# Kernel optimization log

Measured on AMD Instinct MI355X. Metric: run time of the kernel, lower is better.

The kernel has to match this reference:

```python
import jax, jax.numpy as jnp
import numpy as np

EPS = 1e-5

def _face_normals(v, vi):
    # v: [B,V,3], vi: [F,3] -> [B,F,3]
    pts = v[:, vi]                                  # [B,F,3,3]
    n = jnp.cross(pts[:, :, 1] - pts[:, :, 0], pts[:, :, 2] - pts[:, :, 0])
    norm = jnp.linalg.norm(n, axis=-1, keepdims=True)
    return n / jnp.where(norm < EPS, 1.0, norm)

def _vert_normals(v, vi):
    fn = _face_normals(v, vi)                       # [B,F,3]
    fn_rep = jnp.repeat(fn, 3, axis=1)              # [B,3F,3] (one copy per face vertex)
    vn = jnp.zeros_like(v).at[:, vi.reshape(-1)].add(fn_rep)
    norm = jnp.linalg.norm(vn, axis=-1, keepdims=True)
    return vn / jnp.where(norm < EPS, 1.0, norm)

def _values_to_uv(values, index_image, bary_image):
    # values: [B,V,C]; index_image/bary_image: [U,U,3] -> [B,C,U,U]
    mask = jnp.all(index_image != -1, axis=-1)      # [U,U]
    idx = jnp.clip(index_image, 0, values.shape[1] - 1)
    vals = values[:, idx]                           # [B,U,U,3,C]
    uv = jnp.einsum('buvkc,uvk->bcuv', vals, bary_image.astype(values.dtype))
    return uv * mask[None, None].astype(values.dtype)

def _grid_sample_bilinear(img, gx, gy):
    # img: [B,C,H,W]; gx,gy: [N] in [-1,1]; align_corners=False, zero padding
    B, C, H, W = img.shape
    ix = ((gx + 1.0) * W - 1.0) * 0.5
    iy = ((gy + 1.0) * H - 1.0) * 0.5
    x0 = jnp.floor(ix); y0 = jnp.floor(iy)
    x1 = x0 + 1.0;      y1 = y0 + 1.0
    wx1 = ix - x0; wx0 = 1.0 - wx1
    wy1 = iy - y0; wy0 = 1.0 - wy1
    def gather(xi, yi):
        valid = (xi >= 0) & (xi < W) & (yi >= 0) & (yi < H)
        xc = jnp.clip(xi, 0, W - 1).astype(jnp.int32)
        yc = jnp.clip(yi, 0, H - 1).astype(jnp.int32)
        return img[:, :, yc, xc] * valid.astype(img.dtype)  # [B,C,N]
    return (gather(x0, y0) * (wx0 * wy0) + gather(x1, y0) * (wx1 * wy0)
          + gather(x0, y1) * (wx0 * wy1) + gather(x1, y1) * (wx1 * wy1))

def _sample_uv(values_uv, uv_coords, v2uv):
    g = uv_coords * 2.0 - 1.0                       # [T,2]
    vals = _grid_sample_bilinear(values_uv, g[:, 0], g[:, 1])  # [B,C,T]
    vals = jnp.transpose(vals, (0, 2, 1))           # [B,T,C]
    return vals[:, v2uv].mean(axis=2)               # [B,V,C]

def setup_inputs() -> dict:
    key = jax.random.key(0)
    ks = jax.random.split(key, 6)
    B, V, Fc, U, T, K = 8, 100000, 200000, 1024, 110000, 2
    verts = jax.random.normal(ks[0], (B, V, 3), jnp.float32)
    vi = jax.random.randint(ks[1], (Fc, 3), 0, V, dtype=jnp.int32)
    index_image = jax.random.randint(ks[2], (U, U, 3), 0, V, dtype=jnp.int32)
    bary_image = jax.random.uniform(ks[3], (U, U, 3), jnp.float32)
    vt = jax.random.uniform(ks[4], (T, 2), jnp.float32)
    v2uv = jax.random.randint(ks[5], (V, K), 0, T, dtype=jnp.int32)
    return {"verts": verts, "bary_image": bary_image, "vt": vt,
            "vi": vi, "index_image": index_image, "v2uv": v2uv}

def reference(verts, bary_image, vt, vi, index_image, v2uv):
    vn = _vert_normals(verts, vi)                   # [B,V,3]
    uv = _values_to_uv(vn, index_image, bary_image) # [B,3,U,U]
    return _sample_uv(uv, vt, v2uv)                 # [B,V,3]
```

## Files before the change

kernel.cpp:

```cpp
#include <hip/hip_runtime.h>

#define EPS 1e-5f

constexpr int B = 8;
constexpr int V = 100000;
constexpr int F = 200000;
constexpr int U = 1024;
constexpr int T = 110000;
constexpr int CAP = 24;

constexpr int TRB = (V + 255) / 256;
constexpr int CZB = (V + 255) / 256;

constexpr int N4   = (3 * F) / 4;
constexpr int ELLB = (N4 + 255) / 256;
constexpr int FNB  = (F * 8 + 255) / 256;
constexpr int CPB  = (T + 255) / 256;
constexpr int PERIODS = ELLB;
constexpr int K2N = PERIODS * 17;

__global__ void k1_pre(const float* __restrict__ verts,
                       float4* __restrict__ vertsT,
                       int* __restrict__ cnt) {
    int blk = blockIdx.x;
    if (blk < TRB) {
        int v = blk * 256 + threadIdx.x;
        if (v >= V) return;
        float4 row[8];
#pragma unroll
        for (int b = 0; b < 8; ++b) {
            const float* p = verts + (size_t)b * V * 3 + (size_t)v * 3;
            row[b] = make_float4(p[0], p[1], p[2], 0.0f);
        }
        float4* dst = vertsT + (size_t)v * 8;
#pragma unroll
        for (int b = 0; b < 8; ++b) dst[b] = row[b];
    } else {
        int i = (blk - TRB) * 256 + threadIdx.x;
        if (i < V) cnt[i] = 0;
    }
}

__global__ void k2_fused(const int* __restrict__ vi,
                         int* __restrict__ cnt,
                         int* __restrict__ ell,
                         const float4* __restrict__ vertsT,
                         float4* __restrict__ fn,
                         const int* __restrict__ index_image,
                         const float* __restrict__ bary_image,
                         const float* __restrict__ vt,
                         int4* __restrict__ cI,
                         float4* __restrict__ cW) {
    int p = blockIdx.x / 17;
    int s = blockIdx.x % 17;

    if (s == 0) {
        int m4 = p * 256 + threadIdx.x;
        if (m4 >= N4) return;
        const int4* vi4 = (const int4*)vi;
        int4 e = vi4[m4];
        int base = m4 * 4;
        int vv[4] = {e.x, e.y, e.z, e.w};
#pragma unroll
        for (int j = 0; j < 4; ++j) {
            int v = vv[j];
            int pos = atomicAdd(&cnt[v], 1);
            if (pos < CAP) ell[v * CAP + pos] = (base + j) / 3;
        }
        return;
    }

    if (s <= 15) {
        int bid = p * 15 + (s - 1);
        if (bid >= FNB) return;
        int id = bid * 256 + threadIdx.x;
        if (id >= F * 8) return;
        int f = id >> 3;
        int b = id & 7;

        int i0 = vi[f * 3 + 0];
        int i1 = vi[f * 3 + 1];
        int i2 = vi[f * 3 + 2];

        float4 p0 = vertsT[(size_t)i0 * 8 + b];
        float4 p1 = vertsT[(size_t)i1 * 8 + b];
        float4 p2 = vertsT[(size_t)i2 * 8 + b];

        float e1x = p1.x - p0.x, e1y = p1.y - p0.y, e1z = p1.z - p0.z;
        float e2x = p2.x - p0.x, e2y = p2.y - p0.y, e2z = p2.z - p0.z;

        float nx = e1y * e2z - e1z * e2y;
        float ny = e1z * e2x - e1x * e2z;
        float nz = e1x * e2y - e1y * e2x;

        float norm = sqrtf(nx * nx + ny * ny + nz * nz);
        float inv = (norm < EPS) ? 1.0f : (1.0f / norm);
        fn[id] = make_float4(nx * inv, ny * inv, nz * inv, 0.0f);
        return;
    }

    if (p >= CPB) return;
    int t = p * 256 + threadIdx.x;
    if (t >= T) return;

    float gx = vt[t * 2 + 0];
    float gy = vt[t * 2 + 1];
    float ix = gx * (float)U - 0.5f;
    float iy = gy * (float)U - 0.5f;

    float x0f = floorf(ix);
    float y0f = floorf(iy);
    int x0 = (int)x0f;
    int y0 = (int)y0f;
    float wx1 = ix - x0f, wx0 = 1.0f - wx1;
    float wy1 = iy - y0f, wy0 = 1.0f - wy1;

#pragma unroll
    for (int c = 0; c < 4; ++c) {
        int cy = c >> 1, cx = c & 1;
        int y = y0 + cy;
        int x = x0 + cx;
        int4 ci = make_int4(0, 0, 0, 0);
        float4 cw = make_float4(0.0f, 0.0f, 0.0f, 0.0f);
        if (x >= 0 && x < U && y >= 0 && y < U) {
            float w = (cy ? wy1 : wy0) * (cx ? wx1 : wx0);
            int pix = y * U + x;
            int i0 = index_image[pix * 3 + 0];
            int i1 = index_image[pix * 3 + 1];
            int i2 = index_image[pix * 3 + 2];
            float m = (i0 != -1 && i1 != -1 && i2 != -1) ? 1.0f : 0.0f;
            float wm = w * m;
            ci.x = min(max(i0, 0), V - 1);
            ci.y = min(max(i1, 0), V - 1);
            ci.z = min(max(i2, 0), V - 1);
            cw.x = wm * bary_image[pix * 3 + 0];
            cw.y = wm * bary_image[pix * 3 + 1];
            cw.z = wm * bary_image[pix * 3 + 2];
        }
        cI[t * 4 + c] = ci;
        cW[t * 4 + c] = cw;
    }
}

__global__ void gather_vn(const float4* __restrict__ fn,
                          const int* __restrict__ cnt,
                          const int* __restrict__ ell,
                          float4* __restrict__ vn) {
    int id = blockIdx.x * blockDim.x + threadIdx.x;
    if (id >= V * 8) return;
    int v = id >> 3;
    int b = id & 7;

    int deg = min(cnt[v], CAP);
    const int* row = ell + (size_t)v * CAP;

    float ax = 0.0f, ay = 0.0f, az = 0.0f;
    for (int j = 0; j < deg; ++j) {
        int f = row[j];
        float4 n = fn[(size_t)f * 8 + b];
        ax += n.x; ay += n.y; az += n.z;
    }

    float n = sqrtf(ax * ax + ay * ay + az * az);
    float inv = (n < EPS) ? 1.0f : (1.0f / n);
    vn[id] = make_float4(ax * inv, ay * inv, az * inv, 0.0f);
}

__global__ void sample_points(const float4* __restrict__ vn,
                              const int4* __restrict__ cI,
                              const float4* __restrict__ cW,
                              float4* __restrict__ vals) {
    int id = blockIdx.x * blockDim.x + threadIdx.x;
    if (id >= T * 8) return;
    int t = id >> 3;
    int b = id & 7;

    float ax = 0.0f, ay = 0.0f, az = 0.0f;
#pragma unroll
    for (int c = 0; c < 4; ++c) {
        int4 ci = cI[t * 4 + c];
        float4 cw = cW[t * 4 + c];
        float4 q0 = vn[(size_t)ci.x * 8 + b];
        float4 q1 = vn[(size_t)ci.y * 8 + b];
        float4 q2 = vn[(size_t)ci.z * 8 + b];
        ax += cw.x * q0.x + cw.y * q1.x + cw.z * q2.x;
        ay += cw.x * q0.y + cw.y * q1.y + cw.z * q2.y;
        az += cw.x * q0.z + cw.y * q1.z + cw.z * q2.z;
    }

    vals[id] = make_float4(ax, ay, az, 0.0f);
}

__global__ void gather_out(const float4* __restrict__ vals,
                           const int* __restrict__ v2uv,
                           float* __restrict__ out) {
    int id = blockIdx.x * blockDim.x + threadIdx.x;
    if (id >= V * 8) return;
    int v = id >> 3;
    int b = id & 7;

    int t0 = v2uv[v * 2 + 0];
    int t1 = v2uv[v * 2 + 1];
    float4 x = vals[(size_t)t0 * 8 + b];
    float4 y = vals[(size_t)t1 * 8 + b];

    float* o = out + (size_t)b * V * 3 + (size_t)v * 3;
    o[0] = 0.5f * (x.x + y.x);
    o[1] = 0.5f * (x.y + y.y);
    o[2] = 0.5f * (x.z + y.z);
}

extern "C" void kernel_launch(void* const* d_in, const int* in_sizes, int n_in,
                              void* d_out, int out_size, void* d_ws, size_t ws_size,
                              hipStream_t stream) {
    const float* verts   = (const float*)d_in[0];
    const float* bary    = (const float*)d_in[1];
    const float* vt      = (const float*)d_in[2];
    const int*   vi      = (const int*)d_in[3];
    const int*   idx_img = (const int*)d_in[4];
    const int*   v2uv    = (const int*)d_in[5];
    float* out = (float*)d_out;

    float4* vertsT = (float4*)d_ws;
    float4* vn     = vertsT;
    float4* fn     = vertsT + (size_t)V * 8;
    float4* vals   = fn;
    int4*   cI     = (int4*)(fn + (size_t)F * 8);
    float4* cW     = (float4*)(cI + (size_t)T * 4);
    int*    cnt    = (int*)(cW + (size_t)T * 4);
    int*    ell    = cnt + V;

    const int BLK = 256;
    k1_pre<<<TRB + CZB, BLK, 0, stream>>>(verts, vertsT, cnt);
    k2_fused<<<K2N, BLK, 0, stream>>>(
        vi, cnt, ell, vertsT, fn, idx_img, bary, vt, cI, cW);
    gather_vn<<<(V * 8 + BLK - 1) / BLK, BLK, 0, stream>>>(fn, cnt, ell, vn);
    sample_points<<<(T * 8 + BLK - 1) / BLK, BLK, 0, stream>>>(vn, cI, cW, vals);
    gather_out<<<(V * 8 + BLK - 1) / BLK, BLK, 0, stream>>>(vals, v2uv, out);
}
```

Before: 195.9 us.

## Replace global-atomic ELL build with bucketed counting-sort adjacency and shared-memory gather

Replaces the per-vertex global atomicAdd ELL construction with a two-pass bucketed counting sort. Per-block shared-memory histograms are built over 128-vertex buckets, scanned into offsets, and used to scatter packed (local vertex, face) pairs. Each bucket block then rebuilds its adjacency rows in shared memory and gathers the face normals. This removes contended global atomics and scattered ELL writes, at the cost of two extra kernel launches, a serial single-block scan, and nondeterministic face ordering within rows.

```diff
diff --git a/kernel.cpp b/kernel.cpp
--- a/kernel.cpp
+++ b/kernel.cpp
@@ -9,19 +9,18 @@
 constexpr int T = 110000;
 constexpr int CAP = 24;
 
-constexpr int TRB = (V + 255) / 256;
-constexpr int CZB = (V + 255) / 256;
-
+constexpr int NBUK = (V + 127) / 128;
 constexpr int N4   = (3 * F) / 4;
-constexpr int ELLB = (N4 + 255) / 256;
+constexpr int EB   = (N4 + 255) / 256;
+constexpr int TRB  = (V + 255) / 256;
 constexpr int FNB  = (F * 8 + 255) / 256;
 constexpr int CPB  = (T + 255) / 256;
-constexpr int PERIODS = ELLB;
-constexpr int K2N = PERIODS * 17;
 
 __global__ void k1_pre(const float* __restrict__ verts,
                        float4* __restrict__ vertsT,
-                       int* __restrict__ cnt) {
+                       const int* __restrict__ vi,
+                       int* __restrict__ hist) {
+    __shared__ int lh[NBUK];
     int blk = blockIdx.x;
     if (blk < TRB) {
         int v = blk * 256 + threadIdx.x;
@@ -36,44 +35,36 @@
 #pragma unroll
         for (int b = 0; b < 8; ++b) dst[b] = row[b];
     } else {
-        int i = (blk - TRB) * 256 + threadIdx.x;
-        if (i < V) cnt[i] = 0;
+        int k = blk - TRB;
+        for (int i = threadIdx.x; i < NBUK; i += 256) lh[i] = 0;
+        __syncthreads();
+        int m4 = k * 256 + threadIdx.x;
+        if (m4 < N4) {
+            int4 e = ((const int4*)vi)[m4];
+            atomicAdd(&lh[e.x >> 7], 1);
+            atomicAdd(&lh[e.y >> 7], 1);
+            atomicAdd(&lh[e.z >> 7], 1);
+            atomicAdd(&lh[e.w >> 7], 1);
+        }
+        __syncthreads();
+        for (int b = threadIdx.x; b < NBUK; b += 256) hist[k * NBUK + b] = lh[b];
     }
 }
 
 __global__ void k2_fused(const int* __restrict__ vi,
-                         int* __restrict__ cnt,
-                         int* __restrict__ ell,
                          const float4* __restrict__ vertsT,
                          float4* __restrict__ fn,
                          const int* __restrict__ index_image,
                          const float* __restrict__ bary_image,
                          const float* __restrict__ vt,
                          int4* __restrict__ cI,
-                         float4* __restrict__ cW) {
-    int p = blockIdx.x / 17;
-    int s = blockIdx.x % 17;
-
-    if (s == 0) {
-        int m4 = p * 256 + threadIdx.x;
-        if (m4 >= N4) return;
-        const int4* vi4 = (const int4*)vi;
-        int4 e = vi4[m4];
-        int base = m4 * 4;
-        int vv[4] = {e.x, e.y, e.z, e.w};
-#pragma unroll
-        for (int j = 0; j < 4; ++j) {
-            int v = vv[j];
-            int pos = atomicAdd(&cnt[v], 1);
-            if (pos < CAP) ell[v * CAP + pos] = (base + j) / 3;
-        }
-        return;
-    }
-
-    if (s <= 15) {
-        int bid = p * 15 + (s - 1);
-        if (bid >= FNB) return;
-        int id = bid * 256 + threadIdx.x;
+                         float4* __restrict__ cW,
+                         int* __restrict__ hist,
+                         int* __restrict__ tot) {
+    int blk = blockIdx.x;
+
+    if (blk < FNB) {
+        int id = blk * 256 + threadIdx.x;
         if (id >= F * 8) return;
         int f = id >> 3;
         int b = id & 7;
@@ -99,71 +90,150 @@
         return;
     }
 
-    if (p >= CPB) return;
-    int t = p * 256 + threadIdx.x;
-    if (t >= T) return;
-
-    float gx = vt[t * 2 + 0];
-    float gy = vt[t * 2 + 1];
-    float ix = gx * (float)U - 0.5f;
-    float iy = gy * (float)U - 0.5f;
-
-    float x0f = floorf(ix);
-    float y0f = floorf(iy);
-    int x0 = (int)x0f;
-    int y0 = (int)y0f;
-    float wx1 = ix - x0f, wx0 = 1.0f - wx1;
-    float wy1 = iy - y0f, wy0 = 1.0f - wy1;
-
-#pragma unroll
-    for (int c = 0; c < 4; ++c) {
-        int cy = c >> 1, cx = c & 1;
-        int y = y0 + cy;
-        int x = x0 + cx;
-        int4 ci = make_int4(0, 0, 0, 0);
-        float4 cw = make_float4(0.0f, 0.0f, 0.0f, 0.0f);
-        if (x >= 0 && x < U && y >= 0 && y < U) {
-            float w = (cy ? wy1 : wy0) * (cx ? wx1 : wx0);
-            int pix = y * U + x;
-            int i0 = index_image[pix * 3 + 0];
-            int i1 = index_image[pix * 3 + 1];
-            int i2 = index_image[pix * 3 + 2];
-            float m = (i0 != -1 && i1 != -1 && i2 != -1) ? 1.0f : 0.0f;
-            float wm = w * m;
-            ci.x = min(max(i0, 0), V - 1);
-            ci.y = min(max(i1, 0), V - 1);
-            ci.z = min(max(i2, 0), V - 1);
-            cw.x = wm * bary_image[pix * 3 + 0];
-            cw.y = wm * bary_image[pix * 3 + 1];
-            cw.z = wm * bary_image[pix * 3 + 2];
-        }
-        cI[t * 4 + c] = ci;
-        cW[t * 4 + c] = cw;
-    }
-}
-
-__global__ void gather_vn(const float4* __restrict__ fn,
-                          const int* __restrict__ cnt,
-                          const int* __restrict__ ell,
-                          float4* __restrict__ vn) {
-    int id = blockIdx.x * blockDim.x + threadIdx.x;
-    if (id >= V * 8) return;
-    int v = id >> 3;
-    int b = id & 7;
-
-    int deg = min(cnt[v], CAP);
-    const int* row = ell + (size_t)v * CAP;
-
-    float ax = 0.0f, ay = 0.0f, az = 0.0f;
-    for (int j = 0; j < deg; ++j) {
-        int f = row[j];
-        float4 n = fn[(size_t)f * 8 + b];
-        ax += n.x; ay += n.y; az += n.z;
-    }
-
-    float n = sqrtf(ax * ax + ay * ay + az * az);
-    float inv = (n < EPS) ? 1.0f : (1.0f / n);
-    vn[id] = make_float4(ax * inv, ay * inv, az * inv, 0.0f);
+    if (blk < FNB + CPB) {
+        int t = (blk - FNB) * 256 + threadIdx.x;
+        if (t >= T) return;
+
+        float gx = vt[t * 2 + 0];
+        float gy = vt[t * 2 + 1];
+        float ix = gx * (float)U - 0.5f;
+        float iy = gy * (float)U - 0.5f;
+
+        float x0f = floorf(ix);
+        float y0f = floorf(iy);
+        int x0 = (int)x0f;
+        int y0 = (int)y0f;
+        float wx1 = ix - x0f, wx0 = 1.0f - wx1;
+        float wy1 = iy - y0f, wy0 = 1.0f - wy1;
+
+#pragma unroll
+        for (int c = 0; c < 4; ++c) {
+            int cy = c >> 1, cx = c & 1;
+            int y = y0 + cy;
+            int x = x0 + cx;
+            int4 ci = make_int4(0, 0, 0, 0);
+            float4 cw = make_float4(0.0f, 0.0f, 0.0f, 0.0f);
+            if (x >= 0 && x < U && y >= 0 && y < U) {
+                float w = (cy ? wy1 : wy0) * (cx ? wx1 : wx0);
+                int pix = y * U + x;
+                int i0 = index_image[pix * 3 + 0];
+                int i1 = index_image[pix * 3 + 1];
+                int i2 = index_image[pix * 3 + 2];
+                float m = (i0 != -1 && i1 != -1 && i2 != -1) ? 1.0f : 0.0f;
+                float wm = w * m;
+                ci.x = min(max(i0, 0), V - 1);
+                ci.y = min(max(i1, 0), V - 1);
+                ci.z = min(max(i2, 0), V - 1);
+                cw.x = wm * bary_image[pix * 3 + 0];
+                cw.y = wm * bary_image[pix * 3 + 1];
+                cw.z = wm * bary_image[pix * 3 + 2];
+            }
+            cI[t * 4 + c] = ci;
+            cW[t * 4 + c] = cw;
+        }
+        return;
+    }
+
+    {
+        __shared__ int part[256];
+        int b = blk - FNB - CPB;
+        int th = threadIdx.x;
+        int k0 = th * 3;
+        int c0 = (k0     < EB) ? hist[(k0    ) * NBUK + b] : 0;
+        int c1 = (k0 + 1 < EB) ? hist[(k0 + 1) * NBUK + b] : 0;
+        int c2 = (k0 + 2 < EB) ? hist[(k0 + 2) * NBUK + b] : 0;
+        int local = c0 + c1 + c2;
+        part[th] = local;
+        __syncthreads();
+        for (int off = 1; off < 256; off <<= 1) {
+            int x = (th >= off) ? part[th - off] : 0;
+            __syncthreads();
+            part[th] += x;
+            __syncthreads();
+        }
+        int excl = part[th] - local;
+        if (th == 255) tot[b] = part[255];
+        if (k0     < EB) hist[(k0    ) * NBUK + b] = excl;
+        if (k0 + 1 < EB) hist[(k0 + 1) * NBUK + b] = excl + c0;
+        if (k0 + 2 < EB) hist[(k0 + 2) * NBUK + b] = excl + c0 + c1;
+    }
+}
+
+__global__ void k3_base(const int* __restrict__ tot, int* __restrict__ base) {
+    __shared__ int s[1024];
+    int t = threadIdx.x;
+    int c = (t < NBUK) ? tot[t] : 0;
+    s[t] = c;
+    __syncthreads();
+    for (int off = 1; off < 1024; off <<= 1) {
+        int x = (t >= off) ? s[t - off] : 0;
+        __syncthreads();
+        s[t] += x;
+        __syncthreads();
+    }
+    if (t <= NBUK) base[t] = s[t] - c;
+}
+
+__global__ void k4_scatter(const int* __restrict__ vi,
+                           const int* __restrict__ off,
+                           const int* __restrict__ base,
+                           int* __restrict__ pairs) {
+    __shared__ int lh[NBUK];
+    int k = blockIdx.x;
+    for (int i = threadIdx.x; i < NBUK; i += 256) lh[i] = 0;
+    __syncthreads();
+    int m4 = k * 256 + threadIdx.x;
+    if (m4 >= N4) return;
+    int4 e = ((const int4*)vi)[m4];
+    int be = m4 * 4;
+    int vv[4] = {e.x, e.y, e.z, e.w};
+#pragma unroll
+    for (int j = 0; j < 4; ++j) {
+        int v = vv[j];
+        int b = v >> 7;
+        int r = atomicAdd(&lh[b], 1);
+        int pos = base[b] + off[k * NBUK + b] + r;
+        pairs[pos] = ((v & 127) << 18) | ((be + j) / 3);
+    }
+}
+
+__global__ __launch_bounds__(512) void k5_gather(
+        const int* __restrict__ pairs,
+        const int* __restrict__ base,
+        const float4* __restrict__ fn,
+        float4* __restrict__ vn) {
+    __shared__ int cnt[128];
+    __shared__ int rows[128 * CAP];
+    int b = blockIdx.x;
+    int tid = threadIdx.x;
+    if (tid < 128) cnt[tid] = 0;
+    __syncthreads();
+
+    int start = base[b], end = base[b + 1];
+    for (int i = start + tid; i < end; i += 512) {
+        int pk = pairs[i];
+        int vl = pk >> 18;
+        int f = pk & 0x3FFFF;
+        int pos = atomicAdd(&cnt[vl], 1);
+        if (pos < CAP) rows[vl * CAP + pos] = f;
+    }
+    __syncthreads();
+
+    int v0 = b << 7;
+    for (int id = tid; id < 128 * 8; id += 512) {
+        int vl = id >> 3, b8 = id & 7;
+        int v = v0 + vl;
+        if (v >= V) continue;
+        int deg = min(cnt[vl], CAP);
+        float ax = 0.0f, ay = 0.0f, az = 0.0f;
+        for (int j = 0; j < deg; ++j) {
+            float4 n = fn[(size_t)rows[vl * CAP + j] * 8 + b8];
+            ax += n.x; ay += n.y; az += n.z;
+        }
+        float nn = sqrtf(ax * ax + ay * ay + az * az);
+        float inv = (nn < EPS) ? 1.0f : (1.0f / nn);
+        vn[(size_t)v * 8 + b8] = make_float4(ax * inv, ay * inv, az * inv, 0.0f);
+    }
 }
 
 __global__ void sample_points(const float4* __restrict__ vn,
@@ -227,14 +297,18 @@
     float4* vals   = fn;
     int4*   cI     = (int4*)(fn + (size_t)F * 8);
     float4* cW     = (float4*)(cI + (size_t)T * 4);
-    int*    cnt    = (int*)(cW + (size_t)T * 4);
-    int*    ell    = cnt + V;
+    int*    hist   = (int*)(cW + (size_t)T * 4);
+    int*    tot    = hist + (size_t)EB * NBUK;
+    int*    base   = tot + NBUK;
+    int*    pairs  = base + NBUK + 1;
 
     const int BLK = 256;
-    k1_pre<<<TRB + CZB, BLK, 0, stream>>>(verts, vertsT, cnt);
-    k2_fused<<<K2N, BLK, 0, stream>>>(
-        vi, cnt, ell, vertsT, fn, idx_img, bary, vt, cI, cW);
-    gather_vn<<<(V * 8 + BLK - 1) / BLK, BLK, 0, stream>>>(fn, cnt, ell, vn);
+    k1_pre<<<TRB + EB, BLK, 0, stream>>>(verts, vertsT, vi, hist);
+    k2_fused<<<FNB + CPB + NBUK, BLK, 0, stream>>>(
+        vi, vertsT, fn, idx_img, bary, vt, cI, cW, hist, tot);
+    k3_base<<<1, 1024, 0, stream>>>(tot, base);
+    k4_scatter<<<EB, BLK, 0, stream>>>(vi, hist, base, pairs);
+    k5_gather<<<NBUK, 512, 0, stream>>>(pairs, base, fn, vn);
     sample_points<<<(T * 8 + BLK - 1) / BLK, BLK, 0, stream>>>(vn, cI, cW, vals);
     gather_out<<<(V * 8 + BLK - 1) / BLK, BLK, 0, stream>>>(vals, v2uv, out);
 }
```

Measured after the change: 199.3 us. No clear change (+1.8%).
